# Performance work log

Measured on AMD Instinct MI355X. Metric: run time of the kernel, lower is better.

## Reference

```python
import jax, jax.numpy as jnp
import numpy as np

F_SIZE = 1000   # feature_size
FIELDS = 39     # field_size
K = 40          # ffm embedding dim
BATCH = 4096
LAYERS = [1024, 512, 256]


def setup_inputs() -> dict:
    key = jax.random.key(0)
    ks = jax.random.split(key, 12)
    inp = {
        "X": jax.random.normal(ks[0], (BATCH, F_SIZE), dtype=jnp.float32),
        "w1": jax.random.normal(ks[1], (F_SIZE,), dtype=jnp.float32) * 0.01,
        "b": jnp.full((1,), 0.5, dtype=jnp.float32),
        "nfk": jax.random.normal(ks[2], (F_SIZE, FIELDS, K), dtype=jnp.float32) * 0.01,
        "f2f": jax.random.randint(ks[3], (F_SIZE,), 0, FIELDS, dtype=jnp.int32),
    }
    dims = [F_SIZE] + LAYERS
    for i in range(len(LAYERS)):
        fan_in, fan_out = dims[i], dims[i + 1]
        scale = np.sqrt(6.0 / (fan_in + fan_out)).astype(np.float32)
        inp[f"deepW{i}"] = jax.random.uniform(ks[4 + i], (fan_in, fan_out), dtype=jnp.float32, minval=-scale, maxval=scale)
        inp[f"deepB{i}"] = jnp.zeros((fan_out,), dtype=jnp.float32)
    scale = np.sqrt(6.0 / (LAYERS[-1] + 1)).astype(np.float32)
    inp["outW"] = jax.random.uniform(ks[10], (LAYERS[-1], 1), dtype=jnp.float32, minval=-scale, maxval=scale)
    inp["outB"] = jnp.zeros((1,), dtype=jnp.float32)
    return inp


def reference(X, w1, b, nfk, f2f, deepW0, deepB0, deepW1, deepB1, deepW2, deepB2, outW, outB):
    # --- linear term: sum_i w1[i]*X[:,i] + b ---
    linear = X @ w1 + b[0]                                  # [B]

    # --- field-aware interaction ---
    # A[i, j, :] = nfk[i, f2f[j], :]  (gather over fields)
    F = nfk.shape[0]
    A = nfk[jnp.arange(F)[:, None], f2f[None, :], :]        # [F, F, K]
    # S[i, j] = <nfk[i, f2f[j]], nfk[j, f2f[i]]> -- batch-independent scalar
    S = jnp.einsum('ijk,jik->ij', A, A)                     # [F, F]
    M = jnp.triu(S, 1)                                      # keep i < j pairs only
    # sum_{i<j} S[i,j] * X[:,i] * X[:,j]
    interaction = jnp.sum((X @ M) * X, axis=1)              # [B]

    # --- deep part (train=False: no dropout) ---
    h = jax.nn.relu(X @ deepW0 + deepB0)
    h = jax.nn.relu(h @ deepW1 + deepB1)
    h = jax.nn.relu(h @ deepW2 + deepB2)
    deep = (h @ outW + outB).reshape(-1)                    # [B]

    out_sum = linear + interaction + deep                   # logits [B]
    return out_sum
```

## Files before the change

### kernel.cpp

```cpp
#include <hip/hip_runtime.h>


#define BATCH   4096
#define FSZ     1000
#define NFIELDS 39
#define KDIM    40

typedef __attribute__((ext_vector_type(8))) short short8v;
typedef __attribute__((ext_vector_type(4))) float f32x4;

__device__ __forceinline__ short f2bf(float f) {
  unsigned u = __builtin_bit_cast(unsigned, f);
  u += 0x7fff + ((u >> 16) & 1);
  return (short)(u >> 16);
}

typedef const __attribute__((address_space(1))) unsigned int* gas_ptr;
typedef __attribute__((address_space(3))) unsigned int* las_ptr;
__device__ __forceinline__ void gload16(const void* g, void* l) {
  __builtin_amdgcn_global_load_lds((gas_ptr)g, (las_ptr)l, 16, 0, 0);
}

__device__ __forceinline__ void transp32(
    const float* __restrict__ in, short* __restrict__ out, int idx, int nx,
    int K_in, int N_in, int Kpad, float (*t)[33], int tid)
{
  int n0 = (idx % nx) * 32, k0 = (idx / nx) * 32;
  int tx = tid & 31, ty = tid >> 5;
  #pragma unroll
  for (int i = 0; i < 32; i += 8) {
    int k = k0 + ty + i, n = n0 + tx;
    t[ty + i][tx] = (k < K_in && n < N_in) ? in[(size_t)k * N_in + n] : 0.f;
  }
  __syncthreads();
  #pragma unroll
  for (int i = 0; i < 32; i += 8) {
    int n = n0 + ty + i, k = k0 + tx;
    if (n < N_in && k < Kpad) out[(size_t)n * Kpad + k] = f2bf(t[tx][ty + i]);
  }
}

__global__ __launch_bounds__(256) void prep_kernel(
    const float* __restrict__ X, const float* __restrict__ nfk,
    const int* __restrict__ f2f,
    const float* __restrict__ W0, const float* __restrict__ W1,
    const float* __restrict__ W2,
    short* __restrict__ Xb, short* __restrict__ B12,
    short* __restrict__ Wt1, short* __restrict__ Wt2)
{
  __shared__ float tbuf[32][33];
  const int bid = blockIdx.x, tid = threadIdx.x;
  if (bid < 4096) {
    int k = tid * 4;
    short4 o = make_short4(0, 0, 0, 0);
    if (k < FSZ) {
      float4 v = *(const float4*)(X + (size_t)bid * FSZ + k);
      o = make_short4(f2bf(v.x), f2bf(v.y), f2bf(v.z), f2bf(v.w));
    }
    *(short4*)(Xb + (size_t)bid * 1024 + k) = o;
  } else if (bid < 8192) {
    int idx = bid - 4096;
    int n = idx >> 2, k = (idx & 3) * 256 + tid;
    float s = 0.f;
    if (n < FSZ && k < FSZ && n > k) {
      int fn = f2f[n], fk = f2f[k];
      const float4* p = (const float4*)(nfk + ((size_t)k * NFIELDS + fn) * KDIM);
      const float4* q = (const float4*)(nfk + ((size_t)n * NFIELDS + fk) * KDIM);
      #pragma unroll
      for (int t = 0; t < KDIM / 4; ++t) {
        float4 a = p[t], b = q[t];
        s += a.x * b.x + a.y * b.y + a.z * b.z + a.w * b.w;
      }
    }
    B12[(size_t)n * 1024 + k] = f2bf(s);
  } else if (bid < 9216) {
    transp32(W0, B12 + 1024 * 1024, bid - 8192, 32, 1000, 1024, 1024, tbuf, tid);
  } else if (bid < 9728) {
    transp32(W1, Wt1, bid - 9216, 16, 1024, 512, 1024, tbuf, tid);
  } else {
    transp32(W2, Wt2, bid - 9728, 8, 512, 256, 512, tbuf, tid);
  }
}

template<int BM, int BN, int EPI>
__global__ __launch_bounds__(256) void gemm_mfma(
    const short* __restrict__ A, const short* __restrict__ Bt,
    const float* __restrict__ bias, void* __restrict__ Cout,
    int N, int K,
    const float* __restrict__ X, const float* __restrict__ w1,
    float* __restrict__ partial)
{
  constexpr int AM = BM / 32, AN = BN / 32;
  __shared__ __align__(16) short As[2][BM * 64];
  __shared__ __align__(16) short Bs[2][BN * 64];
  __shared__ float pbuf[2][128];

  const int tid  = threadIdx.x;
  const int wid  = tid >> 6;
  const int lane = tid & 63;
  const int wr   = wid >> 1, wc = wid & 1;
  const int row0 = blockIdx.y * BM;
  const int col0 = blockIdx.x * BN;

  const int lr8   = lane >> 3;
  const int cbase = (lane & 7) * 16;

  f32x4 acc[AM][AN];
  #pragma unroll
  for (int m = 0; m < AM; ++m)
    #pragma unroll
    for (int n = 0; n < AN; ++n) acc[m][n] = (f32x4)(0.f);

  auto stage = [&](int p, int k0) {
    #pragma unroll
    for (int j = 0; j < BM / 32; ++j) {
      int i = j * 4 + wid;
      int r = i * 8 + lr8;
      int cb = cbase ^ ((r & 7) << 4);
      gload16((const char*)A + (((size_t)(row0 + r) * K + k0) << 1) + cb,
              (char*)&As[p][0] + i * 1024);
    }
    #pragma unroll
    for (int j = 0; j < BN / 32; ++j) {
      int i = j * 4 + wid;
      int r = i * 8 + lr8;
      int cb = cbase ^ ((r & 7) << 4);
      gload16((const char*)Bt + (((size_t)(col0 + r) * K + k0) << 1) + cb,
              (char*)&Bs[p][0] + i * 1024);
    }
  };

  auto compute = [&](int p) {
    #pragma unroll
    for (int kk = 0; kk < 2; ++kk) {
      const int cb = kk * 64 + (lane >> 4) * 16;
      short8v a[AM], b[AN];
      #pragma unroll
      for (int m = 0; m < AM; ++m) {
        int r = wr * (BM / 2) + m * 16 + (lane & 15);
        a[m] = *(const short8v*)((const char*)&As[p][0] + r * 128 + (cb ^ ((r & 7) << 4)));
      }
      #pragma unroll
      for (int n = 0; n < AN; ++n) {
        int r = wc * (BN / 2) + n * 16 + (lane & 15);
        b[n] = *(const short8v*)((const char*)&Bs[p][0] + r * 128 + (cb ^ ((r & 7) << 4)));
      }
      #pragma unroll
      for (int m = 0; m < AM; ++m)
        #pragma unroll
        for (int n = 0; n < AN; ++n)
          acc[m][n] = __builtin_amdgcn_mfma_f32_16x16x32_bf16(a[m], b[n], acc[m][n], 0, 0, 0);
    }
  };

  const int nt = K >> 6;
  stage(0, 0);
  __syncthreads();
  for (int t = 0; t < nt; ++t) {
    if (t + 1 < nt) stage((t + 1) & 1, (t + 1) << 6);
    compute(t & 1);
    __syncthreads();
  }

  const int cr = (lane >> 4) * 4;
  const int cc = lane & 15;

  if (EPI == 0) {
    if (blockIdx.x < 8) {
      float rsum[AM * 4];
      #pragma unroll
      for (int i = 0; i < AM * 4; ++i) rsum[i] = 0.f;
      #pragma unroll
      for (int m = 0; m < AM; ++m) {
        #pragma unroll
        for (int n = 0; n < AN; ++n) {
          int gc = col0 + wc * (BN / 2) + n * 16 + cc;
          bool ok = gc < FSZ;
          float w1v = ok ? w1[gc] : 0.f;
          #pragma unroll
          for (int r = 0; r < 4; ++r) {
            int gr = row0 + wr * (BM / 2) + m * 16 + cr + r;
            float xv = ok ? X[(size_t)gr * FSZ + gc] : 0.f;
            rsum[m * 4 + r] = fmaf(acc[m][n][r] + w1v, xv, rsum[m * 4 + r]);
          }
        }
      }
      #pragma unroll
      for (int mask = 1; mask < 16; mask <<= 1)
        #pragma unroll
        for (int i = 0; i < AM * 4; ++i)
          rsum[i] += __shfl_xor(rsum[i], mask, 64);
      if (cc == 0) {
        #pragma unroll
        for (int m = 0; m < AM; ++m)
          #pragma unroll
          for (int r = 0; r < 4; ++r)
            pbuf[wc][wr * (BM / 2) + m * 16 + cr + r] = rsum[m * 4 + r];
      }
      __syncthreads();
      if (tid < BM)
        partial[(size_t)(row0 + tid) * 8 + blockIdx.x] = pbuf[0][tid] + pbuf[1][tid];
    } else {
      #pragma unroll
      for (int m = 0; m < AM; ++m) {
        #pragma unroll
        for (int n = 0; n < AN; ++n) {
          int gc = col0 - 1024 + wc * (BN / 2) + n * 16 + cc;
          float bv = bias[gc];
          #pragma unroll
          for (int r = 0; r < 4; ++r) {
            int gr = row0 + wr * (BM / 2) + m * 16 + cr + r;
            float v = fmaxf(acc[m][n][r] + bv, 0.f);
            ((short*)Cout)[(size_t)gr * 1024 + gc] = f2bf(v);
          }
        }
      }
    }
  } else {
    #pragma unroll
    for (int m = 0; m < AM; ++m) {
      #pragma unroll
      for (int n = 0; n < AN; ++n) {
        int gc = col0 + wc * (BN / 2) + n * 16 + cc;
        float bv = bias[gc];
        #pragma unroll
        for (int r = 0; r < 4; ++r) {
          int gr = row0 + wr * (BM / 2) + m * 16 + cr + r;
          float v = fmaxf(acc[m][n][r] + bv, 0.f);
          if (EPI == 1) ((short*)Cout)[(size_t)gr * N + gc] = f2bf(v);
          else          ((float*)Cout)[(size_t)gr * N + gc] = v;
        }
      }
    }
  }
}

__global__ __launch_bounds__(256) void finalize_kernel(
    const float* __restrict__ h2, const float* __restrict__ oW,
    const float* __restrict__ oB, const float* __restrict__ bsc,
    const float* __restrict__ partial, float* __restrict__ out)
{
  __shared__ float sm[4];
  int b = blockIdx.x, t = threadIdx.x;
  float p = h2[(size_t)b * 256 + t] * oW[t];
  if (t < 8) p += partial[(size_t)b * 8 + t];
  #pragma unroll
  for (int o = 32; o; o >>= 1) p += __shfl_down(p, o, 64);
  int lane = t & 63, w = t >> 6;
  if (!lane) sm[w] = p;
  __syncthreads();
  if (!t) out[b] = sm[0] + sm[1] + sm[2] + sm[3] + bsc[0] + oB[0];
}

extern "C" void kernel_launch(void* const* d_in, const int* in_sizes, int n_in,
                              void* d_out, int out_size, void* d_ws, size_t ws_size,
                              hipStream_t stream) {
  const float* X   = (const float*)d_in[0];
  const float* w1  = (const float*)d_in[1];
  const float* bsc = (const float*)d_in[2];
  const float* nfk = (const float*)d_in[3];
  const int*   f2f = (const int*)d_in[4];
  const float* W0  = (const float*)d_in[5];
  const float* B0  = (const float*)d_in[6];
  const float* W1  = (const float*)d_in[7];
  const float* B1  = (const float*)d_in[8];
  const float* W2  = (const float*)d_in[9];
  const float* B2  = (const float*)d_in[10];
  const float* oW  = (const float*)d_in[11];
  const float* oB  = (const float*)d_in[12];
  float* out = (float*)d_out;

  char* ws = (char*)d_ws;
  short* Xb   = (short*)(ws);
  short* B12  = (short*)(ws + 8388608);
  short* Wt1  = (short*)(ws + 12582912);
  short* Wt2  = (short*)(ws + 13631488);
  float* part = (float*)(ws + 13893632);
  short* h0   = (short*)(ws + 14680064);
  short* h1   = (short*)(ws + 23068672);
  float* h2   = (float*)(ws + 27262976);

  prep_kernel<<<9856, 256, 0, stream>>>(X, nfk, f2f, W0, W1, W2,
                                        Xb, B12, Wt1, Wt2);
  gemm_mfma<128, 128, 0><<<dim3(16, 32), 256, 0, stream>>>(
      Xb, B12, B0, h0, 2048, 1024, X, w1, part);
  gemm_mfma<64, 128, 1><<<dim3(4, 64), 256, 0, stream>>>(
      h0, Wt1, B1, h1, 512, 1024, nullptr, nullptr, nullptr);
  gemm_mfma<64, 64, 2><<<dim3(4, 64), 256, 0, stream>>>(
      h1, Wt2, B2, h2, 256, 512, nullptr, nullptr, nullptr);
  finalize_kernel<<<BATCH, 256, 0, stream>>>(h2, oW, oB, bsc, part, out);
}
```

Baseline: 87.17 us.

## Fuse output projection into last GEMM and truncate K loop for triangular interaction

After: 83.74 us. 3.9% less time.

```diff
diff --git a/kernel.cpp b/kernel.cpp
--- a/kernel.cpp
+++ b/kernel.cpp
@@ -93,7 +93,7 @@
   constexpr int AM = BM / 32, AN = BN / 32;
   __shared__ __align__(16) short As[2][BM * 64];
   __shared__ __align__(16) short Bs[2][BN * 64];
-  __shared__ float pbuf[2][128];
+  __shared__ float pbuf[2][BM];
 
   const int tid  = threadIdx.x;
   const int wid  = tid >> 6;
@@ -153,7 +153,12 @@
     }
   };
 
-  const int nt = K >> 6;
+  int nt = K >> 6;
+  if (EPI == 0 && blockIdx.x < 8) {
+    int need = ((int)blockIdx.x * 2) + 2;
+    nt = nt < need ? nt : need;
+  }
+
   stage(0, 0);
   __syncthreads();
   for (int t = 0; t < nt; ++t) {
@@ -216,7 +221,7 @@
         }
       }
     }
-  } else {
+  } else if (EPI == 1) {
     #pragma unroll
     for (int m = 0; m < AM; ++m) {
       #pragma unroll
@@ -227,29 +232,57 @@
         for (int r = 0; r < 4; ++r) {
           int gr = row0 + wr * (BM / 2) + m * 16 + cr + r;
           float v = fmaxf(acc[m][n][r] + bv, 0.f);
-          if (EPI == 1) ((short*)Cout)[(size_t)gr * N + gc] = f2bf(v);
-          else          ((float*)Cout)[(size_t)gr * N + gc] = v;
+          ((short*)Cout)[(size_t)gr * N + gc] = f2bf(v);
         }
       }
     }
+  } else {
+    float rsum[AM * 4];
+    #pragma unroll
+    for (int i = 0; i < AM * 4; ++i) rsum[i] = 0.f;
+    #pragma unroll
+    for (int m = 0; m < AM; ++m) {
+      #pragma unroll
+      for (int n = 0; n < AN; ++n) {
+        int gc = col0 + wc * (BN / 2) + n * 16 + cc;
+        float bv = bias[gc];
+        float ow = w1[gc];
+        #pragma unroll
+        for (int r = 0; r < 4; ++r) {
+          float v = fmaxf(acc[m][n][r] + bv, 0.f);
+          rsum[m * 4 + r] = fmaf(v, ow, rsum[m * 4 + r]);
+        }
+      }
+    }
+    #pragma unroll
+    for (int mask = 1; mask < 16; mask <<= 1)
+      #pragma unroll
+      for (int i = 0; i < AM * 4; ++i)
+        rsum[i] += __shfl_xor(rsum[i], mask, 64);
+    if (cc == 0) {
+      #pragma unroll
+      for (int m = 0; m < AM; ++m)
+        #pragma unroll
+        for (int r = 0; r < 4; ++r)
+          pbuf[wc][wr * (BM / 2) + m * 16 + cr + r] = rsum[m * 4 + r];
+    }
+    __syncthreads();
+    if (tid < BM)
+      partial[(size_t)(row0 + tid) * 4 + blockIdx.x] = pbuf[0][tid] + pbuf[1][tid];
   }
 }
 
 __global__ __launch_bounds__(256) void finalize_kernel(
-    const float* __restrict__ h2, const float* __restrict__ oW,
-    const float* __restrict__ oB, const float* __restrict__ bsc,
-    const float* __restrict__ partial, float* __restrict__ out)
+    const float* __restrict__ part, const float* __restrict__ part2,
+    const float* __restrict__ bsc, const float* __restrict__ oB,
+    float* __restrict__ out)
 {
-  __shared__ float sm[4];
-  int b = blockIdx.x, t = threadIdx.x;
-  float p = h2[(size_t)b * 256 + t] * oW[t];
-  if (t < 8) p += partial[(size_t)b * 8 + t];
-  #pragma unroll
-  for (int o = 32; o; o >>= 1) p += __shfl_down(p, o, 64);
-  int lane = t & 63, w = t >> 6;
-  if (!lane) sm[w] = p;
-  __syncthreads();
-  if (!t) out[b] = sm[0] + sm[1] + sm[2] + sm[3] + bsc[0] + oB[0];
+  int b = blockIdx.x * 256 + threadIdx.x;
+  const float4* p = (const float4*)(part + (size_t)b * 8);
+  float4 a = p[0], c = p[1];
+  float4 d = *(const float4*)(part2 + (size_t)b * 4);
+  out[b] = a.x + a.y + a.z + a.w + c.x + c.y + c.z + c.w
+         + d.x + d.y + d.z + d.w + bsc[0] + oB[0];
 }
 
 extern "C" void kernel_launch(void* const* d_in, const int* in_sizes, int n_in,
@@ -271,14 +304,14 @@
   float* out = (float*)d_out;
 
   char* ws = (char*)d_ws;
-  short* Xb   = (short*)(ws);
-  short* B12  = (short*)(ws + 8388608);
-  short* Wt1  = (short*)(ws + 12582912);
-  short* Wt2  = (short*)(ws + 13631488);
-  float* part = (float*)(ws + 13893632);
-  short* h0   = (short*)(ws + 14680064);
-  short* h1   = (short*)(ws + 23068672);
-  float* h2   = (float*)(ws + 27262976);
+  short* Xb    = (short*)(ws);
+  short* B12   = (short*)(ws + 8388608);
+  short* Wt1   = (short*)(ws + 12582912);
+  short* Wt2   = (short*)(ws + 13631488);
+  float* part  = (float*)(ws + 13893632);
+  float* part2 = (float*)(ws + 14024704);
+  short* h0    = (short*)(ws + 14680064);
+  short* h1    = (short*)(ws + 23068672);
 
   prep_kernel<<<9856, 256, 0, stream>>>(X, nfk, f2f, W0, W1, W2,
                                         Xb, B12, Wt1, Wt2);
@@ -286,7 +319,7 @@
       Xb, B12, B0, h0, 2048, 1024, X, w1, part);
   gemm_mfma<64, 128, 1><<<dim3(4, 64), 256, 0, stream>>>(
       h0, Wt1, B1, h1, 512, 1024, nullptr, nullptr, nullptr);
-  gemm_mfma<64, 64, 2><<<dim3(4, 64), 256, 0, stream>>>(
-      h1, Wt2, B2, h2, 256, 512, nullptr, nullptr, nullptr);
-  finalize_kernel<<<BATCH, 256, 0, stream>>>(h2, oW, oB, bsc, part, out);
-}
+  gemm_mfma<64, 64, 3><<<dim3(4, 64), 256, 0, stream>>>(
+      h1, Wt2, B2, nullptr, 256, 512, nullptr, oW, part2);
+  finalize_kernel<<<16, 256, 0, stream>>>(part, part2, bsc, oB, out);
+}
```
